# Kernel tuning notes

Measured on AMD Instinct MI355X. Metric: run time of the kernel, lower is better.

## Reference

```python
import jax, jax.numpy as jnp
import numpy as np

N_NODES = 100000
N_EDGES = 1600000
IN_CH = 128
HID = 128
EPS = 1e-5


def setup_inputs() -> dict:
    key = jax.random.key(0)
    ks = jax.random.split(key, 16)
    x = jax.random.normal(ks[0], (N_NODES, IN_CH), dtype=jnp.float32)
    edge_index = jax.random.randint(ks[1], (2, N_EDGES), 0, N_NODES, dtype=jnp.int64)
    dims = [(IN_CH, HID), (HID, HID), (HID, HID // 2)]
    params = {}
    for i, (di, do) in enumerate(dims):
        params[f'w{i}'] = jax.random.normal(ks[2 + i], (di, do), dtype=jnp.float32) * (1.0 / np.sqrt(di))
        params[f'b{i}'] = jnp.zeros((do,), dtype=jnp.float32)
        params[f'g{i}'] = jnp.ones((do,), dtype=jnp.float32)
        params[f'be{i}'] = jnp.zeros((do,), dtype=jnp.float32)
    params['wc1'] = jax.random.normal(ks[8], (HID // 2, 32), dtype=jnp.float32) * (1.0 / np.sqrt(HID // 2))
    params['bc1'] = jnp.zeros((32,), dtype=jnp.float32)
    params['wc2'] = jax.random.normal(ks[9], (32, 1), dtype=jnp.float32) * (1.0 / np.sqrt(32))
    params['bc2'] = jnp.zeros((1,), dtype=jnp.float32)
    return {'x': x, 'edge_index': edge_index, **params}


def _gcn_forward(x, edge_index, w0, b0, g0, be0, w1, b1, g1, be1, w2, b2, g2, be2, wc1, bc1, wc2, bc2):
    n = x.shape[0]
    # add self-loops (GCNConv default)
    loops = jnp.arange(n, dtype=edge_index.dtype)
    src = jnp.concatenate([edge_index[0], loops])  # [E+N]
    dst = jnp.concatenate([edge_index[1], loops])
    # symmetric normalization: deg over targets (incl. self loops)
    deg = jax.ops.segment_sum(jnp.ones_like(dst, dtype=x.dtype), dst, num_segments=n)
    dis = jax.lax.rsqrt(jnp.maximum(deg, 1e-12))  # deg>=1 due to self loops
    norm = (dis[src] * dis[dst])[:, None]  # [E+N, 1]

    def layer(h, w, b, g, be):
        h = h @ w                                   # [N, d_out]
        h = jax.ops.segment_sum(h[src] * norm, dst, num_segments=n) + b
        mu = jnp.mean(h, axis=0)
        var = jnp.mean(jnp.square(h - mu), axis=0)  # biased var (torch BN)
        h = (h - mu) * jax.lax.rsqrt(var + EPS) * g + be
        return jax.nn.relu(h)                       # dropout: identity (eval)

    h = layer(x, w0, b0, g0, be0)
    h = layer(h, w1, b1, g1, be1)
    h = layer(h, w2, b2, g2, be2)
    h = jax.nn.relu(h @ wc1 + bc1)
    return (h @ wc2 + bc2)[:, 0]  # [N]


def reference(x, edge_index, w0, b0, g0, be0, w1, b1, g1, be1, w2, b2, g2, be2, wc1, bc1, wc2, bc2):
    return _gcn_forward(x, edge_index, w0, b0, g0, be0, w1, b1, g1, be1, w2, b2, g2, be2, wc1, bc1, wc2, bc2)
```

## Files before the change

### kernel.cpp

```cpp
#include <hip/hip_runtime.h>


typedef __attribute__((ext_vector_type(8))) short short8;
typedef __attribute__((ext_vector_type(4))) float f32x4;

#define BIN_SHIFT 7
#define BIN_NODES 128
#define CAPB 4096
#define CAP 64
#define SPARTS 1024

__device__ __forceinline__ float b2f(unsigned short u) {
    return __uint_as_float(((unsigned)u) << 16);
}
__device__ __forceinline__ unsigned short f2bf(float f) {
    unsigned u = __float_as_uint(f);
    return (unsigned short)((u + 0x7fff + ((u >> 16) & 1)) >> 16);
}

__global__ __launch_bounds__(256) void part1_kernel(const int* __restrict__ eidx,
                                                    int E, int nbins, int chunk,
                                                    int* __restrict__ bin_fill,
                                                    int* __restrict__ binned) {
    __shared__ int cntS[1024];
    __shared__ int baseS[1024];
    int tid = threadIdx.x;
    for (int b = tid; b < nbins; b += 256) cntS[b] = 0;
    __syncthreads();
    int e0 = blockIdx.x * chunk;
    int e1 = min(e0 + chunk, E);
    for (int e = e0 + tid; e < e1; e += 256)
        atomicAdd(&cntS[eidx[E + e] >> BIN_SHIFT], 1);
    __syncthreads();
    for (int b = tid; b < nbins; b += 256) {
        baseS[b] = atomicAdd(&bin_fill[b], cntS[b]);
        cntS[b] = 0;
    }
    __syncthreads();
    for (int e = e0 + tid; e < e1; e += 256) {
        int d = eidx[E + e];
        int s = eidx[e];
        int b = d >> BIN_SHIFT;
        int p = baseS[b] + atomicAdd(&cntS[b], 1);
        if (p < CAPB) binned[b * CAPB + p] = (s << BIN_SHIFT) | (d & (BIN_NODES - 1));
    }
}

__global__ __launch_bounds__(256) void part2_kernel(const int* __restrict__ bin_fill,
                                                    const int* __restrict__ binned,
                                                    int N, int* __restrict__ fill,
                                                    float* __restrict__ dis,
                                                    int* __restrict__ stage) {
    __shared__ int lfill[BIN_NODES];
    int b = blockIdx.x, tid = threadIdx.x;
    if (tid < BIN_NODES) lfill[tid] = 0;
    __syncthreads();
    int cnt = min(bin_fill[b], CAPB);
    const int* seg = binned + b * CAPB;
    for (int i = tid; i < cnt; i += 256) {
        int v = seg[i];
        int dl = v & (BIN_NODES - 1);
        int p = atomicAdd(&lfill[dl], 1);
        int node = (b << BIN_SHIFT) + dl;
        if (p < CAP) stage[(node << 6) + p] = v >> BIN_SHIFT;
    }
    __syncthreads();
    if (tid < BIN_NODES) {
        int node = (b << BIN_SHIFT) + tid;
        if (node < N) {
            int c = lfill[tid];
            fill[node] = c;
            dis[node] = rsqrtf((float)c + 1.0f);
        }
    }
}

__global__ void wfrag_kernel(const float* __restrict__ w0,
                             const float* __restrict__ w1,
                             const float* __restrict__ w2,
                             unsigned short* __restrict__ wf) {
    int tid = blockIdx.x * 256 + threadIdx.x;
    if (tid >= 40960) return;
    const float* w;
    int idx, C;
    if (tid < 16384) { w = w0; idx = tid; C = 128; }
    else if (tid < 32768) { w = w1; idx = tid - 16384; C = 128; }
    else { w = w2; idx = tid - 32768; C = 64; }
    int j = idx & 7;
    int lane = (idx >> 3) & 63;
    int q = (idx >> 9) & 3;
    int n_tile = idx >> 11;
    int k = q * 32 + (lane >> 4) * 8 + j;
    int n = n_tile * 16 + (lane & 15);
    wf[tid] = f2bf(w[k * C + n]);
}

__device__ __forceinline__ void load8(const float* p, float4& lo, float4& hi) {
    lo = *(const float4*)p;
    hi = *(const float4*)(p + 4);
}
__device__ __forceinline__ void load8(const unsigned short* p, float4& lo, float4& hi) {
    int4 q = *(const int4*)p;
    lo = make_float4(__uint_as_float((unsigned)q.x << 16),
                     __uint_as_float((unsigned)q.x & 0xffff0000u),
                     __uint_as_float((unsigned)q.y << 16),
                     __uint_as_float((unsigned)q.y & 0xffff0000u));
    hi = make_float4(__uint_as_float((unsigned)q.z << 16),
                     __uint_as_float((unsigned)q.z & 0xffff0000u),
                     __uint_as_float((unsigned)q.w << 16),
                     __uint_as_float((unsigned)q.w & 0xffff0000u));
}

template <int C, typename InT>
__global__ __launch_bounds__(256, 5) void mfma_gemm_kernel(
    const InT* __restrict__ xin, const unsigned short* __restrict__ wf,
    const float* __restrict__ scale, const float* __restrict__ shift,
    const float* __restrict__ dis, unsigned short* __restrict__ out, int N) {
    constexpr int NT = C / 16;
    constexpr int WFRAGS = NT * 4 * 64;
    __shared__ short8 ws[WFRAGS];
    int tid = threadIdx.x;
    for (int i = tid; i < WFRAGS; i += 256) ws[i] = ((const short8*)wf)[i];

    int lane = tid & 63;
    int wave = tid >> 6;
    int m0 = blockIdx.x * 64 + wave * 16;
    int r15 = lane & 15, r4 = lane >> 4;
    f32x4 acc[NT];
#pragma unroll
    for (int t = 0; t < NT; t++) acc[t] = (f32x4){0.f, 0.f, 0.f, 0.f};
    int row0 = m0 + r15;
    int row0c = min(row0, N - 1);
    __syncthreads();

#pragma unroll
    for (int q = 0; q < 4; q++) {
        int kb = q * 32 + r4 * 8;
        float4 a0l, a0h;
        load8(xin + (size_t)row0c * 128 + kb, a0l, a0h);
        if (scale) {
            float4 scl = *(const float4*)&scale[kb];
            float4 sch = *(const float4*)&scale[kb + 4];
            float4 shl = *(const float4*)&shift[kb];
            float4 shh = *(const float4*)&shift[kb + 4];
            a0l.x = fmaxf(a0l.x * scl.x + shl.x, 0.f);
            a0l.y = fmaxf(a0l.y * scl.y + shl.y, 0.f);
            a0l.z = fmaxf(a0l.z * scl.z + shl.z, 0.f);
            a0l.w = fmaxf(a0l.w * scl.w + shl.w, 0.f);
            a0h.x = fmaxf(a0h.x * sch.x + shh.x, 0.f);
            a0h.y = fmaxf(a0h.y * sch.y + shh.y, 0.f);
            a0h.z = fmaxf(a0h.z * sch.z + shh.z, 0.f);
            a0h.w = fmaxf(a0h.w * sch.w + shh.w, 0.f);
        }
        short8 a0;
        a0[0] = (short)f2bf(a0l.x); a0[1] = (short)f2bf(a0l.y);
        a0[2] = (short)f2bf(a0l.z); a0[3] = (short)f2bf(a0l.w);
        a0[4] = (short)f2bf(a0h.x); a0[5] = (short)f2bf(a0h.y);
        a0[6] = (short)f2bf(a0h.z); a0[7] = (short)f2bf(a0h.w);
#pragma unroll
        for (int nt = 0; nt < NT; nt++) {
            short8 b = ws[(nt * 4 + q) * 64 + lane];
            acc[nt] = __builtin_amdgcn_mfma_f32_16x16x32_bf16(a0, b, acc[nt], 0, 0, 0);
        }
    }
    float d0r[4];
#pragma unroll
    for (int r = 0; r < 4; r++) {
        int rowa = m0 + r4 * 4 + r;
        d0r[r] = (rowa < N) ? dis[rowa] : 0.f;
    }
#pragma unroll
    for (int nt = 0; nt < NT; nt++) {
        int col = nt * 16 + r15;
#pragma unroll
        for (int r = 0; r < 4; r++) {
            int rowa = m0 + r4 * 4 + r;
            if (rowa < N) out[(size_t)rowa * C + col] = f2bf(acc[nt][r] * d0r[r]);
        }
    }
}

__global__ __launch_bounds__(256) void agg128_kernel(
    const unsigned short* __restrict__ h, const int* __restrict__ fill,
    const int* __restrict__ stage, const float* __restrict__ dis,
    unsigned short* __restrict__ out, int N) {
    int lane = threadIdx.x & 63;
    int node = blockIdx.x * 4 + (threadIdx.x >> 6);
    if (node >= N) return;
    float dn = dis[node];
    ushort2 sv = ((const ushort2*)(h + (size_t)node * 128))[lane];
    float2 acc = make_float2(b2f(sv.x), b2f(sv.y));
    int ne = min(fill[node], CAP);
    int pk = (lane < ne) ? stage[(node << 6) + lane] : 0;
    int j = 0;
    for (; j + 16 <= ne; j += 16) {
        ushort2 a[16];
#pragma unroll
        for (int t = 0; t < 16; t++) {
            int s = __builtin_amdgcn_readlane(pk, j + t);
            a[t] = ((const ushort2*)(h + (size_t)s * 128))[lane];
        }
#pragma unroll
        for (int t = 0; t < 16; t++) { acc.x += b2f(a[t].x); acc.y += b2f(a[t].y); }
    }
    for (; j + 8 <= ne; j += 8) {
        ushort2 a[8];
#pragma unroll
        for (int t = 0; t < 8; t++) {
            int s = __builtin_amdgcn_readlane(pk, j + t);
            a[t] = ((const ushort2*)(h + (size_t)s * 128))[lane];
        }
#pragma unroll
        for (int t = 0; t < 8; t++) { acc.x += b2f(a[t].x); acc.y += b2f(a[t].y); }
    }
    for (; j + 4 <= ne; j += 4) {
        ushort2 a[4];
#pragma unroll
        for (int t = 0; t < 4; t++) {
            int s = __builtin_amdgcn_readlane(pk, j + t);
            a[t] = ((const ushort2*)(h + (size_t)s * 128))[lane];
        }
#pragma unroll
        for (int t = 0; t < 4; t++) { acc.x += b2f(a[t].x); acc.y += b2f(a[t].y); }
    }
    for (; j < ne; j++) {
        int s = __builtin_amdgcn_readlane(pk, j);
        ushort2 a = ((const ushort2*)(h + (size_t)s * 128))[lane];
        acc.x += b2f(a.x);
        acc.y += b2f(a.y);
    }
    ((ushort2*)(out + (size_t)node * 128))[lane] =
        make_ushort2(f2bf(acc.x * dn), f2bf(acc.y * dn));
}

__global__ __launch_bounds__(256) void agg64_kernel(
    const unsigned short* __restrict__ h, const int* __restrict__ fill,
    const int* __restrict__ stage, const float* __restrict__ dis,
    unsigned short* __restrict__ out, int N) {
    int lane = threadIdx.x & 63;
    int node = blockIdx.x * 4 + (threadIdx.x >> 6);
    if (node >= N) return;
    int half = lane >> 5, ch = lane & 31;
    float dn = dis[node];
    float2 acc = make_float2(0.f, 0.f);
    if (half == 0) {
        ushort2 sv = ((const ushort2*)(h + (size_t)node * 64))[ch];
        acc.x = b2f(sv.x);
        acc.y = b2f(sv.y);
    }
    int ne = min(fill[node], CAP);
    int pk = (lane < ne) ? stage[(node << 6) + lane] : 0;
    int j = 0;
    for (; j + 16 <= ne; j += 16) {
        ushort2 a[8];
#pragma unroll
        for (int t = 0; t < 8; t++) {
            int s = __shfl(pk, j + 2 * t + half);
            a[t] = ((const ushort2*)(h + (size_t)s * 64))[ch];
        }
#pragma unroll
        for (int t = 0; t < 8; t++) { acc.x += b2f(a[t].x); acc.y += b2f(a[t].y); }
    }
    for (; j + 8 <= ne; j += 8) {
        ushort2 a[4];
#pragma unroll
        for (int t = 0; t < 4; t++) {
            int s = __shfl(pk, j + 2 * t + half);
            a[t] = ((const ushort2*)(h + (size_t)s * 64))[ch];
        }
#pragma unroll
        for (int t = 0; t < 4; t++) { acc.x += b2f(a[t].x); acc.y += b2f(a[t].y); }
    }
    for (; j < ne; j += 2) {
        int jj = j + half;
        int s = __shfl(pk, jj);
        bool v = jj < ne;
        ushort2 a = ((const ushort2*)(h + (size_t)s * 64))[ch];
        acc.x += v ? b2f(a.x) : 0.f;
        acc.y += v ? b2f(a.y) : 0.f;
    }
    acc.x += __shfl_down(acc.x, 32);
    acc.y += __shfl_down(acc.y, 32);
    if (half == 0)
        ((ushort2*)(out + (size_t)node * 64))[ch] =
            make_ushort2(f2bf(acc.x * dn), f2bf(acc.y * dn));
}

template <int C>
__global__ __launch_bounds__(256) void stats1_kernel(const unsigned short* __restrict__ h,
                                                     int N, float* __restrict__ partials) {
    constexpr int CG = C / 4;
    constexpr int RG = 256 / CG;
    int t = threadIdx.x;
    int cg = t % CG;
    int rg = t / CG;
    float s[4] = {0.f, 0.f, 0.f, 0.f}, q[4] = {0.f, 0.f, 0.f, 0.f};
    for (int n = blockIdx.x * RG + rg; n < N; n += gridDim.x * RG) {
        ushort4 v = *(const ushort4*)&h[(size_t)n * C + cg * 4];
        float f0 = b2f(v.x), f1 = b2f(v.y), f2 = b2f(v.z), f3 = b2f(v.w);
        s[0] += f0; s[1] += f1; s[2] += f2; s[3] += f3;
        q[0] += f0 * f0; q[1] += f1 * f1; q[2] += f2 * f2; q[3] += f3 * f3;
    }
    __shared__ float red[256 * 8];
#pragma unroll
    for (int k = 0; k < 4; k++) {
        red[(rg * CG + cg) * 8 + k] = s[k];
        red[(rg * CG + cg) * 8 + 4 + k] = q[k];
    }
    __syncthreads();
    if (rg == 0) {
#pragma unroll
        for (int w = 1; w < RG; w++)
#pragma unroll
            for (int k = 0; k < 4; k++) {
                s[k] += red[(w * CG + cg) * 8 + k];
                q[k] += red[(w * CG + cg) * 8 + 4 + k];
            }
        float* pb = partials + (size_t)blockIdx.x * 2 * C;
#pragma unroll
        for (int k = 0; k < 4; k++) {
            pb[cg * 4 + k] = s[k];
            pb[C + cg * 4 + k] = q[k];
        }
    }
}

template <int C>
__global__ __launch_bounds__(256) void stats2_kernel(const float* __restrict__ partials,
                                                     const float* __restrict__ g,
                                                     const float* __restrict__ be, int N,
                                                     float* __restrict__ scale,
                                                     float* __restrict__ shift) {
    int c = blockIdx.x;
    int t = threadIdx.x;
    float s = 0.f, q = 0.f;
    for (int b = t; b < SPARTS; b += 256) {
        const float* pb = partials + (size_t)b * 2 * C;
        s += pb[c];
        q += pb[C + c];
    }
    __shared__ float rs[256], rq[256];
    rs[t] = s;
    rq[t] = q;
    __syncthreads();
    for (int d = 128; d > 0; d >>= 1) {
        if (t < d) {
            rs[t] += rs[t + d];
            rq[t] += rq[t + d];
        }
        __syncthreads();
    }
    if (t == 0) {
        float inv_n = 1.0f / (float)N;
        float mean = rs[0] * inv_n;
        float var = rq[0] * inv_n - mean * mean;
        var = var > 0.f ? var : 0.f;
        float sc = g[c] * rsqrtf(var + 1e-5f);
        scale[c] = sc;
        shift[c] = be[c] - mean * sc;
    }
}

__global__ __launch_bounds__(256) void head_kernel(
    const unsigned short* __restrict__ h, const float* __restrict__ scale,
    const float* __restrict__ shift, const float* __restrict__ wc1,
    const float* __restrict__ bc1, const float* __restrict__ wc2,
    const float* __restrict__ bc2, float* __restrict__ out, int N) {
    __shared__ float w1s[64 * 32];
    __shared__ float b1s[32], w2s[32], s2s[64], sh2[64];
    __shared__ float b2s;
    int tid = threadIdx.x;
    for (int i = tid; i < 64 * 32; i += 256) w1s[i] = wc1[i];
    if (tid < 32) { b1s[tid] = bc1[tid]; w2s[tid] = wc2[tid]; }
    if (tid < 64) { s2s[tid] = scale[tid]; sh2[tid] = shift[tid]; }
    if (tid == 0) b2s = bc2[0];
    __syncthreads();
    int n = blockIdx.x * 256 + tid;
    if (n >= N) return;
    float v[64];
#pragma unroll
    for (int k = 0; k < 64; k++) {
        float x = b2f(h[(size_t)n * 64 + k]) * s2s[k] + sh2[k];
        v[k] = x > 0.f ? x : 0.f;
    }
    float o = b2s;
#pragma unroll 2
    for (int j = 0; j < 32; j++) {
        float t = b1s[j];
#pragma unroll
        for (int k = 0; k < 64; k++) t += v[k] * w1s[k * 32 + j];
        t = t > 0.f ? t : 0.f;
        o += t * w2s[j];
    }
    out[n] = o;
}

extern "C" void kernel_launch(void* const* d_in, const int* in_sizes, int n_in,
                              void* d_out, int out_size, void* d_ws, size_t ws_size,
                              hipStream_t stream) {
    const float* x = (const float*)d_in[0];
    const int* eidx = (const int*)d_in[1];
    const float* w0 = (const float*)d_in[2];
    const float* g0 = (const float*)d_in[4];
    const float* be0 = (const float*)d_in[5];
    const float* w1 = (const float*)d_in[6];
    const float* g1 = (const float*)d_in[8];
    const float* be1 = (const float*)d_in[9];
    const float* w2 = (const float*)d_in[10];
    const float* g2 = (const float*)d_in[12];
    const float* be2 = (const float*)d_in[13];
    const float* wc1 = (const float*)d_in[14];
    const float* bc1 = (const float*)d_in[15];
    const float* wc2 = (const float*)d_in[16];
    const float* bc2 = (const float*)d_in[17];

    const int N = in_sizes[0] / 128;
    const int E = in_sizes[1] / 2;
    const int nbins = (N + BIN_NODES - 1) >> BIN_SHIFT;

    char* p = (char*)d_ws;
    auto alloc = [&](size_t bytes) {
        void* r = (void*)p;
        p += (bytes + 255) & ~(size_t)255;
        return r;
    };
    int* bin_fill = (int*)alloc((size_t)nbins * 4);
    size_t zero_bytes = (size_t)(p - (char*)d_ws);
    int* fill = (int*)alloc((size_t)N * 4);
    int* binned = (int*)alloc((size_t)nbins * CAPB * 4);
    int* stage = (int*)alloc((size_t)N * CAP * 4);
    float* dis = (float*)alloc((size_t)N * 4);
    float* ss = (float*)alloc(3 * 256 * 4);
    float* partials = (float*)alloc((size_t)SPARTS * 256 * 4);
    unsigned short* hA = (unsigned short*)alloc((size_t)N * 128 * 2);
    unsigned short* hB = (unsigned short*)alloc((size_t)N * 128 * 2);
    unsigned short* wf = (unsigned short*)alloc(40960 * 2);
    unsigned short* wf0 = wf;
    unsigned short* wf1 = wf + 16384;
    unsigned short* wf2 = wf + 32768;

    float* sc0 = ss, *sh0 = ss + 128;
    float* sc1 = ss + 256, *sh1 = ss + 384;
    float* sc2 = ss + 512, *sh2 = ss + 640;

    hipMemsetAsync(d_ws, 0, zero_bytes, stream);

    wfrag_kernel<<<160, 256, 0, stream>>>(w0, w1, w2, wf);
    int p1_blocks = 256;
    int chunk = (E + p1_blocks - 1) / p1_blocks;
    part1_kernel<<<p1_blocks, 256, 0, stream>>>(eidx, E, nbins, chunk, bin_fill, binned);
    part2_kernel<<<nbins, 256, 0, stream>>>(bin_fill, binned, N, fill, dis, stage);

    int agg_grid = (N + 3) / 4;
    int gemm_grid = (N + 63) / 64;

    mfma_gemm_kernel<128, float><<<gemm_grid, 256, 0, stream>>>(x, wf0, nullptr, nullptr,
                                                                dis, hA, N);
    agg128_kernel<<<agg_grid, 256, 0, stream>>>(hA, fill, stage, dis, hB, N);
    stats1_kernel<128><<<SPARTS, 256, 0, stream>>>(hB, N, partials);
    stats2_kernel<128><<<128, 256, 0, stream>>>(partials, g0, be0, N, sc0, sh0);

    mfma_gemm_kernel<128, unsigned short><<<gemm_grid, 256, 0, stream>>>(
        hB, wf1, sc0, sh0, dis, hA, N);
    agg128_kernel<<<agg_grid, 256, 0, stream>>>(hA, fill, stage, dis, hB, N);
    stats1_kernel<128><<<SPARTS, 256, 0, stream>>>(hB, N, partials);
    stats2_kernel<128><<<128, 256, 0, stream>>>(partials, g1, be1, N, sc1, sh1);

    mfma_gemm_kernel<64, unsigned short><<<gemm_grid, 256, 0, stream>>>(
        hB, wf2, sc1, sh1, dis, hA, N);
    agg64_kernel<<<agg_grid, 256, 0, stream>>>(hA, fill, stage, dis, hB, N);
    stats1_kernel<64><<<SPARTS, 256, 0, stream>>>(hB, N, partials);
    stats2_kernel<64><<<64, 256, 0, stream>>>(partials, g2, be2, N, sc2, sh2);

    head_kernel<<<(N + 255) / 256, 256, 0, stream>>>(hB, sc2, sh2, wc1, bc1, wc2,
                                                     bc2, (float*)d_out, N);
}
```

Before: 432.6 us.

## Fuse BatchNorm statistics into aggregation kernels and split bin fill counters

The per-channel sum and sum-of-squares for BatchNorm are now computed inside the aggregation kernels. Each block reduces its four nodes in shared memory and atomically adds the result into one of 512 partial slots, so the separate stats1 pass that re-read the whole aggregated feature matrix is gone. The edge-binning atomics are also split into 8 sub-counters per bin, each with its own 512-entry sub-segment, to reduce contention on the global fill counters. The cost is extra global float atomics, larger zeroed buffers, and a risk of dropping edges if one sub-segment exceeds its 512-entry capacity.

```diff
diff --git a/kernel.cpp b/kernel.cpp
--- a/kernel.cpp
+++ b/kernel.cpp
@@ -7,8 +7,9 @@
 #define BIN_SHIFT 7
 #define BIN_NODES 128
 #define CAPB 4096
+#define SUBCAP 512
 #define CAP 64
-#define SPARTS 1024
+#define NSLOTS 512
 
 __device__ __forceinline__ float b2f(unsigned short u) {
     return __uint_as_float(((unsigned)u) << 16);
@@ -25,6 +26,7 @@
     __shared__ int cntS[1024];
     __shared__ int baseS[1024];
     int tid = threadIdx.x;
+    int sub = blockIdx.x & 7;
     for (int b = tid; b < nbins; b += 256) cntS[b] = 0;
     __syncthreads();
     int e0 = blockIdx.x * chunk;
@@ -33,7 +35,7 @@
         atomicAdd(&cntS[eidx[E + e] >> BIN_SHIFT], 1);
     __syncthreads();
     for (int b = tid; b < nbins; b += 256) {
-        baseS[b] = atomicAdd(&bin_fill[b], cntS[b]);
+        baseS[b] = atomicAdd(&bin_fill[b * 8 + sub], cntS[b]);
         cntS[b] = 0;
     }
     __syncthreads();
@@ -42,7 +44,8 @@
         int s = eidx[e];
         int b = d >> BIN_SHIFT;
         int p = baseS[b] + atomicAdd(&cntS[b], 1);
-        if (p < CAPB) binned[b * CAPB + p] = (s << BIN_SHIFT) | (d & (BIN_NODES - 1));
+        if (p < SUBCAP)
+            binned[b * CAPB + sub * SUBCAP + p] = (s << BIN_SHIFT) | (d & (BIN_NODES - 1));
     }
 }
 
@@ -55,14 +58,16 @@
     int b = blockIdx.x, tid = threadIdx.x;
     if (tid < BIN_NODES) lfill[tid] = 0;
     __syncthreads();
-    int cnt = min(bin_fill[b], CAPB);
-    const int* seg = binned + b * CAPB;
-    for (int i = tid; i < cnt; i += 256) {
-        int v = seg[i];
-        int dl = v & (BIN_NODES - 1);
-        int p = atomicAdd(&lfill[dl], 1);
-        int node = (b << BIN_SHIFT) + dl;
-        if (p < CAP) stage[(node << 6) + p] = v >> BIN_SHIFT;
+    for (int sub = 0; sub < 8; sub++) {
+        int cnt = min(bin_fill[b * 8 + sub], SUBCAP);
+        const int* seg = binned + b * CAPB + sub * SUBCAP;
+        for (int i = tid; i < cnt; i += 256) {
+            int v = seg[i];
+            int dl = v & (BIN_NODES - 1);
+            int p = atomicAdd(&lfill[dl], 1);
+            int node = (b << BIN_SHIFT) + dl;
+            if (p < CAP) stage[(node << 6) + p] = v >> BIN_SHIFT;
+        }
     }
     __syncthreads();
     if (tid < BIN_NODES) {
@@ -183,145 +188,159 @@
 __global__ __launch_bounds__(256) void agg128_kernel(
     const unsigned short* __restrict__ h, const int* __restrict__ fill,
     const int* __restrict__ stage, const float* __restrict__ dis,
-    unsigned short* __restrict__ out, int N) {
+    unsigned short* __restrict__ out, int N, float* __restrict__ partials) {
     int lane = threadIdx.x & 63;
-    int node = blockIdx.x * 4 + (threadIdx.x >> 6);
-    if (node >= N) return;
-    float dn = dis[node];
-    ushort2 sv = ((const ushort2*)(h + (size_t)node * 128))[lane];
-    float2 acc = make_float2(b2f(sv.x), b2f(sv.y));
-    int ne = min(fill[node], CAP);
-    int pk = (lane < ne) ? stage[(node << 6) + lane] : 0;
-    int j = 0;
-    for (; j + 16 <= ne; j += 16) {
-        ushort2 a[16];
-#pragma unroll
-        for (int t = 0; t < 16; t++) {
-            int s = __builtin_amdgcn_readlane(pk, j + t);
-            a[t] = ((const ushort2*)(h + (size_t)s * 128))[lane];
-        }
-#pragma unroll
-        for (int t = 0; t < 16; t++) { acc.x += b2f(a[t].x); acc.y += b2f(a[t].y); }
-    }
-    for (; j + 8 <= ne; j += 8) {
-        ushort2 a[8];
-#pragma unroll
-        for (int t = 0; t < 8; t++) {
-            int s = __builtin_amdgcn_readlane(pk, j + t);
-            a[t] = ((const ushort2*)(h + (size_t)s * 128))[lane];
-        }
-#pragma unroll
-        for (int t = 0; t < 8; t++) { acc.x += b2f(a[t].x); acc.y += b2f(a[t].y); }
-    }
-    for (; j + 4 <= ne; j += 4) {
-        ushort2 a[4];
-#pragma unroll
-        for (int t = 0; t < 4; t++) {
-            int s = __builtin_amdgcn_readlane(pk, j + t);
-            a[t] = ((const ushort2*)(h + (size_t)s * 128))[lane];
-        }
-#pragma unroll
-        for (int t = 0; t < 4; t++) { acc.x += b2f(a[t].x); acc.y += b2f(a[t].y); }
-    }
-    for (; j < ne; j++) {
-        int s = __builtin_amdgcn_readlane(pk, j);
-        ushort2 a = ((const ushort2*)(h + (size_t)s * 128))[lane];
-        acc.x += b2f(a.x);
-        acc.y += b2f(a.y);
-    }
-    ((ushort2*)(out + (size_t)node * 128))[lane] =
-        make_ushort2(f2bf(acc.x * dn), f2bf(acc.y * dn));
+    int wave = threadIdx.x >> 6;
+    int node = blockIdx.x * 4 + wave;
+    float ax = 0.f, ay = 0.f;
+    if (node < N) {
+        float dn = dis[node];
+        ushort2 sv = ((const ushort2*)(h + (size_t)node * 128))[lane];
+        float2 acc = make_float2(b2f(sv.x), b2f(sv.y));
+        int ne = min(fill[node], CAP);
+        int pk = (lane < ne) ? stage[(node << 6) + lane] : 0;
+        int j = 0;
+        for (; j + 16 <= ne; j += 16) {
+            ushort2 a[16];
+#pragma unroll
+            for (int t = 0; t < 16; t++) {
+                int s = __builtin_amdgcn_readlane(pk, j + t);
+                a[t] = ((const ushort2*)(h + (size_t)s * 128))[lane];
+            }
+#pragma unroll
+            for (int t = 0; t < 16; t++) { acc.x += b2f(a[t].x); acc.y += b2f(a[t].y); }
+        }
+        for (; j + 8 <= ne; j += 8) {
+            ushort2 a[8];
+#pragma unroll
+            for (int t = 0; t < 8; t++) {
+                int s = __builtin_amdgcn_readlane(pk, j + t);
+                a[t] = ((const ushort2*)(h + (size_t)s * 128))[lane];
+            }
+#pragma unroll
+            for (int t = 0; t < 8; t++) { acc.x += b2f(a[t].x); acc.y += b2f(a[t].y); }
+        }
+        for (; j + 4 <= ne; j += 4) {
+            ushort2 a[4];
+#pragma unroll
+            for (int t = 0; t < 4; t++) {
+                int s = __builtin_amdgcn_readlane(pk, j + t);
+                a[t] = ((const ushort2*)(h + (size_t)s * 128))[lane];
+            }
+#pragma unroll
+            for (int t = 0; t < 4; t++) { acc.x += b2f(a[t].x); acc.y += b2f(a[t].y); }
+        }
+        for (; j < ne; j++) {
+            int s = __builtin_amdgcn_readlane(pk, j);
+            ushort2 a = ((const ushort2*)(h + (size_t)s * 128))[lane];
+            acc.x += b2f(a.x);
+            acc.y += b2f(a.y);
+        }
+        ax = acc.x * dn;
+        ay = acc.y * dn;
+        ((ushort2*)(out + (size_t)node * 128))[lane] = make_ushort2(f2bf(ax), f2bf(ay));
+    }
+    __shared__ float red[4][64][4];
+    red[wave][lane][0] = ax;
+    red[wave][lane][1] = ay;
+    red[wave][lane][2] = ax * ax;
+    red[wave][lane][3] = ay * ay;
+    __syncthreads();
+    if (wave == 0) {
+        float s0 = 0.f, s1 = 0.f, s2 = 0.f, s3 = 0.f;
+#pragma unroll
+        for (int w = 0; w < 4; w++) {
+            s0 += red[w][lane][0];
+            s1 += red[w][lane][1];
+            s2 += red[w][lane][2];
+            s3 += red[w][lane][3];
+        }
+        float* pb = partials + (size_t)(blockIdx.x & (NSLOTS - 1)) * 256;
+        atomicAdd(&pb[lane * 2], s0);
+        atomicAdd(&pb[lane * 2 + 1], s1);
+        atomicAdd(&pb[128 + lane * 2], s2);
+        atomicAdd(&pb[128 + lane * 2 + 1], s3);
+    }
 }
 
 __global__ __launch_bounds__(256) void agg64_kernel(
     const unsigned short* __restrict__ h, const int* __restrict__ fill,
     const int* __restrict__ stage, const float* __restrict__ dis,
-    unsigned short* __restrict__ out, int N) {
+    unsigned short* __restrict__ out, int N, float* __restrict__ partials) {
     int lane = threadIdx.x & 63;
-    int node = blockIdx.x * 4 + (threadIdx.x >> 6);
-    if (node >= N) return;
+    int wave = threadIdx.x >> 6;
+    int node = blockIdx.x * 4 + wave;
     int half = lane >> 5, ch = lane & 31;
-    float dn = dis[node];
-    float2 acc = make_float2(0.f, 0.f);
+    float ax = 0.f, ay = 0.f;
+    if (node < N) {
+        float dn = dis[node];
+        float2 acc = make_float2(0.f, 0.f);
+        if (half == 0) {
+            ushort2 sv = ((const ushort2*)(h + (size_t)node * 64))[ch];
+            acc.x = b2f(sv.x);
+            acc.y = b2f(sv.y);
+        }
+        int ne = min(fill[node], CAP);
+        int pk = (lane < ne) ? stage[(node << 6) + lane] : 0;
+        int j = 0;
+        for (; j + 16 <= ne; j += 16) {
+            ushort2 a[8];
+#pragma unroll
+            for (int t = 0; t < 8; t++) {
+                int s = __shfl(pk, j + 2 * t + half);
+                a[t] = ((const ushort2*)(h + (size_t)s * 64))[ch];
+            }
+#pragma unroll
+            for (int t = 0; t < 8; t++) { acc.x += b2f(a[t].x); acc.y += b2f(a[t].y); }
+        }
+        for (; j + 8 <= ne; j += 8) {
+            ushort2 a[4];
+#pragma unroll
+            for (int t = 0; t < 4; t++) {
+                int s = __shfl(pk, j + 2 * t + half);
+                a[t] = ((const ushort2*)(h + (size_t)s * 64))[ch];
+            }
+#pragma unroll
+            for (int t = 0; t < 4; t++) { acc.x += b2f(a[t].x); acc.y += b2f(a[t].y); }
+        }
+        for (; j < ne; j += 2) {
+            int jj = j + half;
+            int s = __shfl(pk, jj);
+            bool v = jj < ne;
+            ushort2 a = ((const ushort2*)(h + (size_t)s * 64))[ch];
+            acc.x += v ? b2f(a.x) : 0.f;
+            acc.y += v ? b2f(a.y) : 0.f;
+        }
+        acc.x += __shfl_down(acc.x, 32);
+        acc.y += __shfl_down(acc.y, 32);
+        if (half == 0) {
+            ax = acc.x * dn;
+            ay = acc.y * dn;
+            ((ushort2*)(out + (size_t)node * 64))[ch] = make_ushort2(f2bf(ax), f2bf(ay));
+        }
+    }
+    __shared__ float red[4][32][4];
     if (half == 0) {
-        ushort2 sv = ((const ushort2*)(h + (size_t)node * 64))[ch];
-        acc.x = b2f(sv.x);
-        acc.y = b2f(sv.y);
-    }
-    int ne = min(fill[node], CAP);
-    int pk = (lane < ne) ? stage[(node << 6) + lane] : 0;
-    int j = 0;
-    for (; j + 16 <= ne; j += 16) {
-        ushort2 a[8];
-#pragma unroll
-        for (int t = 0; t < 8; t++) {
-            int s = __shfl(pk, j + 2 * t + half);
-            a[t] = ((const ushort2*)(h + (size_t)s * 64))[ch];
-        }
-#pragma unroll
-        for (int t = 0; t < 8; t++) { acc.x += b2f(a[t].x); acc.y += b2f(a[t].y); }
-    }
-    for (; j + 8 <= ne; j += 8) {
-        ushort2 a[4];
-#pragma unroll
-        for (int t = 0; t < 4; t++) {
-            int s = __shfl(pk, j + 2 * t + half);
-            a[t] = ((const ushort2*)(h + (size_t)s * 64))[ch];
-        }
-#pragma unroll
-        for (int t = 0; t < 4; t++) { acc.x += b2f(a[t].x); acc.y += b2f(a[t].y); }
-    }
-    for (; j < ne; j += 2) {
-        int jj = j + half;
-        int s = __shfl(pk, jj);
-        bool v = jj < ne;
-        ushort2 a = ((const ushort2*)(h + (size_t)s * 64))[ch];
-        acc.x += v ? b2f(a.x) : 0.f;
-        acc.y += v ? b2f(a.y) : 0.f;
-    }
-    acc.x += __shfl_down(acc.x, 32);
-    acc.y += __shfl_down(acc.y, 32);
-    if (half == 0)
-        ((ushort2*)(out + (size_t)node * 64))[ch] =
-            make_ushort2(f2bf(acc.x * dn), f2bf(acc.y * dn));
-}
-
-template <int C>
-__global__ __launch_bounds__(256) void stats1_kernel(const unsigned short* __restrict__ h,
-                                                     int N, float* __restrict__ partials) {
-    constexpr int CG = C / 4;
-    constexpr int RG = 256 / CG;
-    int t = threadIdx.x;
-    int cg = t % CG;
-    int rg = t / CG;
-    float s[4] = {0.f, 0.f, 0.f, 0.f}, q[4] = {0.f, 0.f, 0.f, 0.f};
-    for (int n = blockIdx.x * RG + rg; n < N; n += gridDim.x * RG) {
-        ushort4 v = *(const ushort4*)&h[(size_t)n * C + cg * 4];
-        float f0 = b2f(v.x), f1 = b2f(v.y), f2 = b2f(v.z), f3 = b2f(v.w);
-        s[0] += f0; s[1] += f1; s[2] += f2; s[3] += f3;
-        q[0] += f0 * f0; q[1] += f1 * f1; q[2] += f2 * f2; q[3] += f3 * f3;
-    }
-    __shared__ float red[256 * 8];
-#pragma unroll
-    for (int k = 0; k < 4; k++) {
-        red[(rg * CG + cg) * 8 + k] = s[k];
-        red[(rg * CG + cg) * 8 + 4 + k] = q[k];
-    }
-    __syncthreads();
-    if (rg == 0) {
-#pragma unroll
-        for (int w = 1; w < RG; w++)
-#pragma unroll
-            for (int k = 0; k < 4; k++) {
-                s[k] += red[(w * CG + cg) * 8 + k];
-                q[k] += red[(w * CG + cg) * 8 + 4 + k];
-            }
-        float* pb = partials + (size_t)blockIdx.x * 2 * C;
-#pragma unroll
-        for (int k = 0; k < 4; k++) {
-            pb[cg * 4 + k] = s[k];
-            pb[C + cg * 4 + k] = q[k];
-        }
+        red[wave][ch][0] = ax;
+        red[wave][ch][1] = ay;
+        red[wave][ch][2] = ax * ax;
+        red[wave][ch][3] = ay * ay;
+    }
+    __syncthreads();
+    if (wave == 0 && half == 0) {
+        float s0 = 0.f, s1 = 0.f, s2 = 0.f, s3 = 0.f;
+#pragma unroll
+        for (int w = 0; w < 4; w++) {
+            s0 += red[w][ch][0];
+            s1 += red[w][ch][1];
+            s2 += red[w][ch][2];
+            s3 += red[w][ch][3];
+        }
+        float* pb = partials + (size_t)(blockIdx.x & (NSLOTS - 1)) * 256;
+        atomicAdd(&pb[ch * 2], s0);
+        atomicAdd(&pb[ch * 2 + 1], s1);
+        atomicAdd(&pb[64 + ch * 2], s2);
+        atomicAdd(&pb[64 + ch * 2 + 1], s3);
     }
 }
 
@@ -334,8 +353,8 @@
     int c = blockIdx.x;
     int t = threadIdx.x;
     float s = 0.f, q = 0.f;
-    for (int b = t; b < SPARTS; b += 256) {
-        const float* pb = partials + (size_t)b * 2 * C;
+    for (int b = t; b < NSLOTS; b += 256) {
+        const float* pb = partials + (size_t)b * 256;
         s += pb[c];
         q += pb[C + c];
     }
@@ -424,14 +443,16 @@
         p += (bytes + 255) & ~(size_t)255;
         return r;
     };
-    int* bin_fill = (int*)alloc((size_t)nbins * 4);
+    int* bin_fill = (int*)alloc((size_t)nbins * 8 * 4);
+    float* pt0 = (float*)alloc((size_t)NSLOTS * 256 * 4);
+    float* pt1 = (float*)alloc((size_t)NSLOTS * 256 * 4);
+    float* pt2 = (float*)alloc((size_t)NSLOTS * 256 * 4);
     size_t zero_bytes = (size_t)(p - (char*)d_ws);
     int* fill = (int*)alloc((size_t)N * 4);
     int* binned = (int*)alloc((size_t)nbins * CAPB * 4);
     int* stage = (int*)alloc((size_t)N * CAP * 4);
     float* dis = (float*)alloc((size_t)N * 4);
     float* ss = (float*)alloc(3 * 256 * 4);
-    float* partials = (float*)alloc((size_t)SPARTS * 256 * 4);
     unsigned short* hA = (unsigned short*)alloc((size_t)N * 128 * 2);
     unsigned short* hB = (unsigned short*)alloc((size_t)N * 128 * 2);
     unsigned short* wf = (unsigned short*)alloc(40960 * 2);
@@ -456,21 +477,18 @@
 
     mfma_gemm_kernel<128, float><<<gemm_grid, 256, 0, stream>>>(x, wf0, nullptr, nullptr,
                                                                 dis, hA, N);
-    agg128_kernel<<<agg_grid, 256, 0, stream>>>(hA, fill, stage, dis, hB, N);
-    stats1_kernel<128><<<SPARTS, 256, 0, stream>>>(hB, N, partials);
-    stats2_kernel<128><<<128, 256, 0, stream>>>(partials, g0, be0, N, sc0, sh0);
+    agg128_kernel<<<agg_grid, 256, 0, stream>>>(hA, fill, stage, dis, hB, N, pt0);
+    stats2_kernel<128><<<128, 256, 0, stream>>>(pt0, g0, be0, N, sc0, sh0);
 
     mfma_gemm_kernel<128, unsigned short><<<gemm_grid, 256, 0, stream>>>(
         hB, wf1, sc0, sh0, dis, hA, N);
-    agg128_kernel<<<agg_grid, 256, 0, stream>>>(hA, fill, stage, dis, hB, N);
-    stats1_kernel<128><<<SPARTS, 256, 0, stream>>>(hB, N, partials);
-    stats2_kernel<128><<<128, 256, 0, stream>>>(partials, g1, be1, N, sc1, sh1);
+    agg128_kernel<<<agg_grid, 256, 0, stream>>>(hA, fill, stage, dis, hB, N, pt1);
+    stats2_kernel<128><<<128, 256, 0, stream>>>(pt1, g1, be1, N, sc1, sh1);
 
     mfma_gemm_kernel<64, unsigned short><<<gemm_grid, 256, 0, stream>>>(
         hB, wf2, sc1, sh1, dis, hA, N);
-    agg64_kernel<<<agg_grid, 256, 0, stream>>>(hA, fill, stage, dis, hB, N);
-    stats1_kernel<64><<<SPARTS, 256, 0, stream>>>(hB, N, partials);
-    stats2_kernel<64><<<64, 256, 0, stream>>>(partials, g2, be2, N, sc2, sh2);
+    agg64_kernel<<<agg_grid, 256, 0, stream>>>(hA, fill, stage, dis, hB, N, pt2);
+    stats2_kernel<64><<<64, 256, 0, stream>>>(pt2, g2, be2, N, sc2, sh2);
 
     head_kernel<<<(N + 255) / 256, 256, 0, stream>>>(hB, sc2, sh2, wc1, bc1, wc2,
                                                      bc2, (float*)d_out, N);
```

Measured after the change: 444.1 us. 1.03x slower.
